# Optimization experiments

Measured on AMD Instinct MI355X. Metric: run time of the kernel, lower is better.

## Reference

```python
import jax, jax.numpy as jnp
import numpy as np

B, N, C, E, K = 2, 1024, 128, 64, 20

def setup_inputs() -> dict:
    key = jax.random.key(0)
    ks = jax.random.split(key, 4)
    x = jax.random.normal(ks[0], (B, N, C), dtype=jnp.float32)
    Wl = jax.random.normal(ks[1], (C, E), dtype=jnp.float32) * 0.05
    Wr = jax.random.normal(ks[2], (C, E), dtype=jnp.float32) * 0.05
    att = jax.random.normal(ks[3], (1, E), dtype=jnp.float32) * 0.1
    bl = jnp.zeros((E,), dtype=jnp.float32)
    br = jnp.zeros((E,), dtype=jnp.float32)
    edge_index = jnp.zeros((2, 1), dtype=jnp.int64)
    batch = jnp.zeros((B * N,), dtype=jnp.int64)
    return {"x": x, "Wl": Wl, "bl": bl, "Wr": Wr, "br": br, "att": att,
            "edge_index": edge_index, "batch": batch}

def reference(x, Wl, bl, Wr, br, att, edge_index, batch):
    # x: [B, N, C]
    b, n, _ = x.shape
    x_l = x @ Wl + bl              # [B, N, E]
    x_r = x @ Wr + br              # [B, N, E]
    # dense pairwise scores: leaky_relu(x_l_i + x_r_j) . att  -> [B, N, N]
    x_cat = jax.nn.leaky_relu(x_l[:, :, None, :] + x_r[:, None, :, :], 0.2)
    alpha = jnp.einsum('bijd,d->bij', x_cat, att[0])
    alpha = jnp.nan_to_num(alpha, nan=0.0, posinf=0.0, neginf=0.0)
    k = min(K, n)
    vals, idx = jax.lax.top_k(alpha, k)            # [B, N, k]
    attention = jax.nn.softmax(vals, axis=-1).reshape(-1)  # [B*N*k]
    # edge index construction (dropout p used only in training; eval = identity)
    offset = (jnp.arange(b) * n)[:, None]                      # [B, 1]
    index_i = jnp.tile(jnp.repeat(jnp.arange(n), k)[None, :], (b, 1)) + offset
    index_j = idx.reshape(b, n * k) + offset
    new_edge_index = jnp.stack([index_i.reshape(-1), index_j.reshape(-1)], axis=0)
    return new_edge_index, attention
```

## Files before the change

### kernel.cpp

```cpp
#include <hip/hip_runtime.h>

#define Bq 2
#define Nq 1024
#define Cq 128
#define Eq 64
#define Kq 20
#define TI 8
#define BNK (Bq * Nq * Kq)
#define NEGF (-3.0e38f)

#define DPP_F(x, ctrl) __int_as_float(__builtin_amdgcn_update_dpp( \
    __float_as_int(x), __float_as_int(x), (ctrl), 0xf, 0xf, false))
#define DPP_I(x, ctrl) __builtin_amdgcn_update_dpp((x), (x), (ctrl), 0xf, 0xf, false)
#define RL_F(x, l) __int_as_float(__builtin_amdgcn_readlane(__float_as_int(x), (l)))
#define RL_I(x, l) __builtin_amdgcn_readlane((x), (l))
#define QP_XOR1 0xB1
#define QP_XOR2 0x4E
#define ROR4    0x124
#define ROR8    0x128

__global__ __launch_bounds__(128) void proj_kernel(
    const float* __restrict__ x, const float* __restrict__ Wl,
    const float* __restrict__ bl, const float* __restrict__ Wr,
    const float* __restrict__ br, const float* __restrict__ att,
    float* __restrict__ xl, float* __restrict__ xrT, float* __restrict__ rdot) {
  const int row = blockIdx.x;
  const int t = threadIdx.x;
  const int e = t & 63;
  const bool left = (t < 64);
  __shared__ float xs[Cq];
  xs[t] = x[(size_t)row * Cq + t];
  __syncthreads();
  const float* __restrict__ W = left ? Wl : Wr;
  float acc = 0.f;
#pragma unroll 8
  for (int c = 0; c < Cq; ++c) acc = fmaf(xs[c], W[c * Eq + e], acc);
  acc += left ? bl[e] : br[e];
  if (left) {
    xl[(size_t)row * Eq + e] = acc;
  } else {
    xrT[(size_t)e * (Bq * Nq) + row] = acc;
    float s = acc * att[e];
    s += DPP_F(s, QP_XOR1);
    s += DPP_F(s, QP_XOR2);
    s += DPP_F(s, ROR4);
    s += DPP_F(s, ROR8);
    const float sd = (RL_F(s, 0) + RL_F(s, 16)) + (RL_F(s, 32) + RL_F(s, 48));
    if (e == 0) rdot[row] = sd;
  }
}

__global__ __launch_bounds__(1024) void attn_kernel(
    const float* __restrict__ xl, const float* __restrict__ xrT,
    const float* __restrict__ rdot, const float* __restrict__ att,
    float* __restrict__ out) {
  const int gi0  = blockIdx.x * TI;
  const int b    = gi0 >> 10;
  const int tid  = threadIdx.x;
  const int lane = tid & 63;
  const int wave = tid >> 6;

  __shared__ float alpha[TI][Nq];
  __shared__ float xls[TI][Eq];

  if (tid < TI * Eq) xls[tid >> 6][tid & 63] = xl[(size_t)gi0 * Eq + tid];
  __syncthreads();

  {
    const int jt = tid & 255;
    const int j0 = jt * 4;
    const int r0 = (tid >> 8) * 2;
    const float4 rd4 = *(const float4*)&rdot[b * Nq + j0];
    float acc0[4], acc1[4];
    acc0[0] = 1.5f * rd4.x; acc0[1] = 1.5f * rd4.y;
    acc0[2] = 1.5f * rd4.z; acc0[3] = 1.5f * rd4.w;
    acc1[0] = acc0[0]; acc1[1] = acc0[1]; acc1[2] = acc0[2]; acc1[3] = acc0[3];

    const float* __restrict__ xrb = xrT + (size_t)b * Nq + j0;
#pragma unroll
    for (int ch = 0; ch < 16; ++ch) {
      const float4 av4 = *(const float4*)&att[ch * 4];
      const float4 xla = *(const float4*)&xls[r0][ch * 4];
      const float4 xlb = *(const float4*)&xls[r0 + 1][ch * 4];
      const float av[4]  = {av4.x, av4.y, av4.z, av4.w};
      const float la[4]  = {xla.x, xla.y, xla.z, xla.w};
      const float lb[4]  = {xlb.x, xlb.y, xlb.z, xlb.w};
#pragma unroll
      for (int dd = 0; dd < 4; ++dd) {
        const float4 xv4 = *(const float4*)&xrb[(size_t)(ch * 4 + dd) * (Bq * Nq)];
        const float xv[4] = {xv4.x, xv4.y, xv4.z, xv4.w};
        const float a = av[dd];
#pragma unroll
        for (int jj = 0; jj < 4; ++jj) {
          acc0[jj] = fmaf(fabsf(la[dd] + xv[jj]), a, acc0[jj]);
          acc1[jj] = fmaf(fabsf(lb[dd] + xv[jj]), a, acc1[jj]);
        }
      }
    }
    *(float4*)&alpha[r0][j0]     = make_float4(acc0[0], acc0[1], acc0[2], acc0[3]);
    *(float4*)&alpha[r0 + 1][j0] = make_float4(acc1[0], acc1[1], acc1[2], acc1[3]);
  }
  __syncthreads();

  if (wave < TI) {
    float vals[16];
#pragma unroll
    for (int s = 0; s < 16; ++s) vals[s] = alpha[wave][lane + 64 * s];

    float lv = vals[0];
    int   pk = lane;
#pragma unroll
    for (int s = 1; s < 16; ++s)
      if (vals[s] > lv) { lv = vals[s]; pk = (s << 6) | lane; }

    float m0 = 0.f, ssum = 0.f, myv = 0.f;
    int myi = 0;
#pragma unroll 1
    for (int round = 0; round < Kq; ++round) {
      float m = lv;
      m = fmaxf(m, DPP_F(m, QP_XOR1));
      m = fmaxf(m, DPP_F(m, QP_XOR2));
      m = fmaxf(m, DPP_F(m, ROR4));
      m = fmaxf(m, DPP_F(m, ROR8));
      const float bv = fmaxf(fmaxf(RL_F(m, 0), RL_F(m, 16)),
                             fmaxf(RL_F(m, 32), RL_F(m, 48)));
      int key = (lv == bv) ? pk : 0x7FFFFFFF;
      key = min(key, DPP_I(key, QP_XOR1));
      key = min(key, DPP_I(key, QP_XOR2));
      key = min(key, DPP_I(key, ROR4));
      key = min(key, DPP_I(key, ROR8));
      const int jsel = min(min(RL_I(key, 0), RL_I(key, 16)),
                           min(RL_I(key, 32), RL_I(key, 48)));
      if (round == 0) m0 = bv;
      ssum += __expf(0.4f * (bv - m0));
      if (lane == round) { myv = bv; myi = jsel; }
      if (lane == (jsel & 63)) {
        const int sk = jsel >> 6;
#pragma unroll
        for (int s = 0; s < 16; ++s)
          if (s == sk) vals[s] = NEGF;
        lv = vals[0]; pk = lane;
#pragma unroll
        for (int s = 1; s < 16; ++s)
          if (vals[s] > lv) { lv = vals[s]; pk = (s << 6) | lane; }
      }
    }

    if (lane < Kq) {
      const int gi = gi0 + wave;
      const float p = __expf(0.4f * (myv - m0)) / ssum;
      const int base = gi * Kq + lane;
      out[base]            = (float)gi;
      out[BNK + base]      = (float)(b * Nq + myi);
      out[2 * BNK + base]  = p;
    }
  }
}

extern "C" void kernel_launch(void* const* d_in, const int* in_sizes, int n_in,
                              void* d_out, int out_size, void* d_ws, size_t ws_size,
                              hipStream_t stream) {
  const float* x   = (const float*)d_in[0];
  const float* Wl  = (const float*)d_in[1];
  const float* bl  = (const float*)d_in[2];
  const float* Wr  = (const float*)d_in[3];
  const float* br  = (const float*)d_in[4];
  const float* att = (const float*)d_in[5];
  float* out = (float*)d_out;

  float* xl   = (float*)d_ws;
  float* xrT  = xl + (size_t)Bq * Nq * Eq;
  float* rdot = xrT + (size_t)Eq * Bq * Nq;

  proj_kernel<<<Bq * Nq, 128, 0, stream>>>(x, Wl, bl, Wr, br, att, xl, xrT, rdot);
  attn_kernel<<<(Bq * Nq) / TI, 1024, 0, stream>>>(xl, xrT, rdot, att, out);
}
```

Baseline: 41.91 us.

## Pack xr in feature-quads and retile score loop with register prefetch

The right projection is now stored in a packed [E/4][BN][4] layout, so each thread loads four consecutive features of one column as a single float4. In the score loop each thread now covers 2 columns by 4 rows instead of 4 columns by 2 rows. The xl rows are read straight from global memory, using a wave-uniform row index, instead of being staged in shared memory, which drops that shared-memory stage and one barrier. Loads for the next chunk are software-prefetched into registers, which raises register pressure and relies on cached broadcast loads of xl.

```diff
diff --git a/kernel.cpp b/kernel.cpp
--- a/kernel.cpp
+++ b/kernel.cpp
@@ -6,6 +6,7 @@
 #define Eq 64
 #define Kq 20
 #define TI 8
+#define BN (Bq * Nq)
 #define BNK (Bq * Nq * Kq)
 #define NEGF (-3.0e38f)
 
@@ -23,7 +24,7 @@
     const float* __restrict__ x, const float* __restrict__ Wl,
     const float* __restrict__ bl, const float* __restrict__ Wr,
     const float* __restrict__ br, const float* __restrict__ att,
-    float* __restrict__ xl, float* __restrict__ xrT, float* __restrict__ rdot) {
+    float* __restrict__ xl, float* __restrict__ xrP, float* __restrict__ rdot) {
   const int row = blockIdx.x;
   const int t = threadIdx.x;
   const int e = t & 63;
@@ -39,7 +40,7 @@
   if (left) {
     xl[(size_t)row * Eq + e] = acc;
   } else {
-    xrT[(size_t)e * (Bq * Nq) + row] = acc;
+    xrP[((size_t)(e >> 2) * BN + row) * 4 + (e & 3)] = acc;
     float s = acc * att[e];
     s += DPP_F(s, QP_XOR1);
     s += DPP_F(s, QP_XOR2);
@@ -51,7 +52,7 @@
 }
 
 __global__ __launch_bounds__(1024) void attn_kernel(
-    const float* __restrict__ xl, const float* __restrict__ xrT,
+    const float* __restrict__ xl, const float* __restrict__ xrP,
     const float* __restrict__ rdot, const float* __restrict__ att,
     float* __restrict__ out) {
   const int gi0  = blockIdx.x * TI;
@@ -61,44 +62,67 @@
   const int wave = tid >> 6;
 
   __shared__ float alpha[TI][Nq];
-  __shared__ float xls[TI][Eq];
-
-  if (tid < TI * Eq) xls[tid >> 6][tid & 63] = xl[(size_t)gi0 * Eq + tid];
-  __syncthreads();
 
   {
-    const int jt = tid & 255;
-    const int j0 = jt * 4;
-    const int r0 = (tid >> 8) * 2;
-    const float4 rd4 = *(const float4*)&rdot[b * Nq + j0];
-    float acc0[4], acc1[4];
-    acc0[0] = 1.5f * rd4.x; acc0[1] = 1.5f * rd4.y;
-    acc0[2] = 1.5f * rd4.z; acc0[3] = 1.5f * rd4.w;
-    acc1[0] = acc0[0]; acc1[1] = acc0[1]; acc1[2] = acc0[2]; acc1[3] = acc0[3];
-
-    const float* __restrict__ xrb = xrT + (size_t)b * Nq + j0;
+    const int jt = tid & 511;
+    const int r0 = __builtin_amdgcn_readfirstlane(tid >> 9) * 4;
+    const float* __restrict__ vb  = xrP + (size_t)(b * Nq + jt) * 4;
+    const float* __restrict__ xlw = xl + (size_t)(gi0 + r0) * Eq;
+
+    const float rd0 = 1.5f * rdot[b * Nq + jt];
+    const float rd1 = 1.5f * rdot[b * Nq + jt + 512];
+    float acc[4][2];
+#pragma unroll
+    for (int r = 0; r < 4; ++r) { acc[r][0] = rd0; acc[r][1] = rd1; }
+
+    float4 nv0 = *(const float4*)(vb);
+    float4 nv1 = *(const float4*)(vb + 512 * 4);
+    float4 na0 = *(const float4*)(xlw);
+    float4 na1 = *(const float4*)(xlw + Eq);
+    float4 na2 = *(const float4*)(xlw + 2 * Eq);
+    float4 na3 = *(const float4*)(xlw + 3 * Eq);
+    float4 nat = *(const float4*)(att);
+
 #pragma unroll
     for (int ch = 0; ch < 16; ++ch) {
-      const float4 av4 = *(const float4*)&att[ch * 4];
-      const float4 xla = *(const float4*)&xls[r0][ch * 4];
-      const float4 xlb = *(const float4*)&xls[r0 + 1][ch * 4];
-      const float av[4]  = {av4.x, av4.y, av4.z, av4.w};
-      const float la[4]  = {xla.x, xla.y, xla.z, xla.w};
-      const float lb[4]  = {xlb.x, xlb.y, xlb.z, xlb.w};
+      const float4 v0 = nv0, v1 = nv1;
+      const float4 a0 = na0, a1 = na1, a2 = na2, a3 = na3, at = nat;
+      if (ch < 15) {
+        vb += BN * 4;
+        nv0 = *(const float4*)(vb);
+        nv1 = *(const float4*)(vb + 512 * 4);
+        na0 = *(const float4*)(xlw + (ch + 1) * 4);
+        na1 = *(const float4*)(xlw + Eq + (ch + 1) * 4);
+        na2 = *(const float4*)(xlw + 2 * Eq + (ch + 1) * 4);
+        na3 = *(const float4*)(xlw + 3 * Eq + (ch + 1) * 4);
+        nat = *(const float4*)(att + (ch + 1) * 4);
+      }
+      const float* v0p = (const float*)&v0;
+      const float* v1p = (const float*)&v1;
+      const float* a0p = (const float*)&a0;
+      const float* a1p = (const float*)&a1;
+      const float* a2p = (const float*)&a2;
+      const float* a3p = (const float*)&a3;
+      const float* atp = (const float*)&at;
 #pragma unroll
       for (int dd = 0; dd < 4; ++dd) {
-        const float4 xv4 = *(const float4*)&xrb[(size_t)(ch * 4 + dd) * (Bq * Nq)];
-        const float xv[4] = {xv4.x, xv4.y, xv4.z, xv4.w};
-        const float a = av[dd];
-#pragma unroll
-        for (int jj = 0; jj < 4; ++jj) {
-          acc0[jj] = fmaf(fabsf(la[dd] + xv[jj]), a, acc0[jj]);
-          acc1[jj] = fmaf(fabsf(lb[dd] + xv[jj]), a, acc1[jj]);
-        }
+        const float a = atp[dd];
+        const float x0 = v0p[dd], x1 = v1p[dd];
+        acc[0][0] = fmaf(fabsf(a0p[dd] + x0), a, acc[0][0]);
+        acc[0][1] = fmaf(fabsf(a0p[dd] + x1), a, acc[0][1]);
+        acc[1][0] = fmaf(fabsf(a1p[dd] + x0), a, acc[1][0]);
+        acc[1][1] = fmaf(fabsf(a1p[dd] + x1), a, acc[1][1]);
+        acc[2][0] = fmaf(fabsf(a2p[dd] + x0), a, acc[2][0]);
+        acc[2][1] = fmaf(fabsf(a2p[dd] + x1), a, acc[2][1]);
+        acc[3][0] = fmaf(fabsf(a3p[dd] + x0), a, acc[3][0]);
+        acc[3][1] = fmaf(fabsf(a3p[dd] + x1), a, acc[3][1]);
       }
     }
-    *(float4*)&alpha[r0][j0]     = make_float4(acc0[0], acc0[1], acc0[2], acc0[3]);
-    *(float4*)&alpha[r0 + 1][j0] = make_float4(acc1[0], acc1[1], acc1[2], acc1[3]);
+#pragma unroll
+    for (int r = 0; r < 4; ++r) {
+      alpha[r0 + r][jt]       = acc[r][0];
+      alpha[r0 + r][jt + 512] = acc[r][1];
+    }
   }
   __syncthreads();
 
@@ -169,9 +193,9 @@
   float* out = (float*)d_out;
 
   float* xl   = (float*)d_ws;
-  float* xrT  = xl + (size_t)Bq * Nq * Eq;
-  float* rdot = xrT + (size_t)Eq * Bq * Nq;
-
-  proj_kernel<<<Bq * Nq, 128, 0, stream>>>(x, Wl, bl, Wr, br, att, xl, xrT, rdot);
-  attn_kernel<<<(Bq * Nq) / TI, 1024, 0, stream>>>(xl, xrT, rdot, att, out);
+  float* xrP  = xl + (size_t)BN * Eq;
+  float* rdot = xrP + (size_t)16 * BN * 4;
+
+  proj_kernel<<<BN, 128, 0, stream>>>(x, Wl, bl, Wr, br, att, xl, xrP, rdot);
+  attn_kernel<<<BN / TI, 1024, 0, stream>>>(xl, xrP, rdot, att, out);
 }
```

Result: faster. 39.43 us (-5.9%).
